# Performance work log

Hardware: AMD Instinct MI355X
Metric: run time of the kernel (lower is better)

The kernel has to match this reference:

```python
import jax, jax.numpy as jnp
import numpy as np

B, H, Wd, CIN = 4, 64, 64, 65   # batch, height, width, in_channels (incl. time)
COUT = 256                      # out_channels (incl. time)
K = 3
KK = K * K
PAD, STRIDE = 1, 1
SOUT = 4                        # output_stabilizer_size (C4 rotations)
CURV = 1.0                      # Lorentz manifold curvature k
LIN_FEAT = (CIN - 1) * KK + 1   # 577


def make_c4_z2_indices(ksize):
    # (out_rotation, in_stabilizer=1, u, v, [s, u_src, v_src]) index table,
    # realizing the C4 filter rotation as a gather (as in GrouPy).
    f = np.arange(ksize * ksize).reshape(ksize, ksize)
    inds = np.zeros((4, 1, ksize, ksize, 3), dtype=np.int64)
    for r in range(4):
        rot = np.rot90(f, r)
        u, v = np.unravel_index(rot, (ksize, ksize))
        inds[r, 0, :, :, 1] = u
        inds[r, 0, :, :, 2] = v
    return inds

INDS = make_c4_z2_indices(K)


def setup_inputs() -> dict:
    key = jax.random.key(0)
    k1, k2, k3 = jax.random.split(key, 3)
    stdv = float(np.sqrt(2.0 / ((CIN - 1) * KK)))  # reset_parameters
    x = jax.random.normal(k1, (B, H, Wd, CIN), dtype=jnp.float32)
    W = jax.random.uniform(k2, (COUT, LIN_FEAT), minval=-stdv, maxval=stdv, dtype=jnp.float32)
    b = jax.random.uniform(k3, (COUT,), minval=-stdv, maxval=stdv, dtype=jnp.float32)
    return {"x": x, "W": W, "b": b}


def _unfold(x):
    # x: (B, C, H, W) -> (B, C*KK, Ho*Wo) in torch.nn.Unfold layout (channel-major, kernel-minor)
    xp = jnp.pad(x, ((0, 0), (0, 0), (PAD, PAD), (PAD, PAD)))
    ho = (H + 2 * PAD - K) // STRIDE + 1
    wo = (Wd + 2 * PAD - K) // STRIDE + 1
    cols = [xp[:, :, i:i + ho * STRIDE:STRIDE, j:j + wo * STRIDE:STRIDE]
            for i in range(K) for j in range(K)]
    p = jnp.stack(cols, axis=2)  # (B, C, KK, ho, wo)
    return p.reshape(B, CIN * KK, ho * wo), ho, wo


def _forward(x, W, b):
    # torch code does x.view(B, C, H, W) on channel-last data: a reshape, not a permute.
    xv = x.reshape(B, CIN, H, Wd)
    patches, ho, wo = _unfold(xv)
    patches = jnp.transpose(patches, (0, 2, 1))          # (B, P, C*KK)
    P = patches.shape[1]
    patches = patches.reshape(B, P, CIN, 1, K, K)
    patches = jnp.broadcast_to(patches, (B, P, CIN, SOUT, K, K))  # repeat over group dim
    # --- group-equivariant filter transform realized as a gather on patches ---
    ir = INDS.reshape(-1, 3)                              # (SOUT*KK, 3)
    pi = patches[:, :, :, ir[:, 0], ir[:, 1], ir[:, 2]]   # (B, P, C, SOUT*KK)
    pi = pi.reshape(B, P, CIN, SOUT, KK)
    pt = jnp.transpose(pi, (3, 0, 1, 2, 4)).reshape(SOUT, B, P, CIN * KK)
    # --- extract_lorentz_patches (vectorized over group dim) ---
    sqrt_k = jnp.sqrt(jnp.float32(CURV))
    t = jnp.maximum(pt[..., :KK], sqrt_k)                 # clamp time components
    t_resc = jnp.sqrt(jnp.sum(t * t, axis=-1, keepdims=True) - (KK - 1) * CURV)
    sp = pt[..., KK:]                                     # (SOUT,B,P,(C-1)*KK) channel-major
    sp = sp.reshape(SOUT, B, P, CIN - 1, KK).swapaxes(-1, -2).reshape(SOUT, B, P, (CIN - 1) * KK)
    pre = jnp.concatenate([t_resc, sp], axis=-1)          # (SOUT,B,P,LIN_FEAT)
    # --- LorentzFullyConnected: linear, then recompute time from space norm ---
    y = jnp.einsum('gbpf,of->gbpo', pre, W) + b           # (SOUT,B,P,COUT)
    y_sp = y[..., 1:]
    y_t = jnp.sqrt(jnp.sum(y_sp * y_sp, axis=-1, keepdims=True) + CURV)
    out = jnp.concatenate([y_t, y_sp], axis=-1)
    out = jnp.transpose(out, (1, 0, 2, 3)).reshape(B, SOUT, ho, wo, COUT)
    return out


def reference(x, W, b):
    return _forward(x, W, b)
```

## Files before the change

### kernel.cpp

```cpp
#include <hip/hip_runtime.h>
#include <hip/hip_bf16.h>

#define CIN 65
#define LIN 577
#define NSTEP 18
#define M_  16384

typedef __bf16 bf16x8 __attribute__((ext_vector_type(8)));
typedef float  f32x4  __attribute__((ext_vector_type(4)));
typedef unsigned short u16x8 __attribute__((ext_vector_type(8)));

__constant__ int SIG[4][9] = {
  {0,1,2,3,4,5,6,7,8},
  {2,5,8,1,4,7,0,3,6},
  {8,7,6,5,4,3,2,1,0},
  {6,3,0,7,4,1,8,5,2}};

__device__ __forceinline__ int swzm(int r) { return (r ^ (r >> 2)) & 3; }

__global__ __launch_bounds__(512) void prep_k(const float* __restrict__ x,
                                              const float* __restrict__ W,
                                              __hip_bfloat16* __restrict__ A,
                                              __hip_bfloat16* __restrict__ Wg,
                                              float* __restrict__ T) {
  __shared__ float lds[CIN * 3 * 72];
  const int tid = threadIdx.x;
  if (blockIdx.x >= 256) {
    int pidx = (blockIdx.x - 256) * 512 + tid;
    int jc  = pidx & 3;
    int col = (pidx >> 2) & 255;
    int t   = pidx >> 10;
    int ks  = t % NSTEP, g = t / NSTEP;
    int k   = SIG[(4 - g) & 3][ks >> 1];
    const float* src = W + col * LIN + 1 + k * 64 + (ks & 1) * 32 + jc * 8;
    u16x8 pk;
#pragma unroll
    for (int e = 0; e < 8; ++e) {
      union { __hip_bfloat16 h; unsigned short u; } cv;
      cv.h = __float2bfloat16(src[e]);
      pk[e] = cv.u;
    }
    *(u16x8*)(Wg + (size_t)pidx * 8) = pk;
    return;
  }
  const int b = blockIdx.x >> 6, py = blockIdx.x & 63;
  const float* xb = x + (size_t)b * (CIN * 4096);
  for (int i = tid; i < CIN * 3 * 18; i += 512)
    *(f32x4*)&lds[i * 4] = (f32x4){0.f, 0.f, 0.f, 0.f};
  __syncthreads();
  for (int i = tid; i < CIN * 3 * 16; i += 512) {
    int pr = i >> 4, j = i & 15;
    int c = pr / 3, dy = pr - c * 3;
    int hy = py + dy - 1;
    if (hy >= 0 && hy < 64)
      *(f32x4*)&lds[c * 216 + dy * 72 + 4 + j * 4] =
          *(const f32x4*)(xb + c * 4096 + hy * 64 + j * 4);
  }
  __syncthreads();

  const int wave = tid >> 6, px = tid & 63;
  const int rowid = (blockIdx.x << 6) | px;
#pragma unroll
  for (int qi = 0; qi < 9; ++qi) {
    int q = wave * 9 + qi;
    int m = q >> 3, cb8 = q & 7;
    int dy = m / 3, dx = m - dy * 3;
    const float* src = &lds[(1 + cb8 * 8) * 216 + dy * 72 + 3 + dx + px];
    u16x8 pk;
#pragma unroll
    for (int e = 0; e < 8; ++e) {
      union { __hip_bfloat16 h; unsigned short u; } cv;
      cv.h = __float2bfloat16(src[e * 216]);
      pk[e] = cv.u;
    }
    *(u16x8*)(A + ((size_t)q * M_ + rowid) * 8) = pk;
  }
  if (wave == 0) {
    float s = 0.f;
#pragma unroll
    for (int m = 0; m < 9; ++m) {
      float t = fmaxf(lds[(m / 3) * 72 + 3 + (m % 3) + px], 1.f);
      s += t * t;
    }
    T[rowid] = sqrtf(s - 8.f);
  }
}

__device__ __forceinline__ void async_cp16(const void* g, void* ldsbase) {
  __builtin_amdgcn_global_load_lds(
      (const __attribute__((address_space(1))) void*)g,
      (__attribute__((address_space(3))) void*)ldsbase, 16, 0, 0);
}

__global__ __launch_bounds__(256, 4) void gemm_k(const __hip_bfloat16* __restrict__ A,
                                                 const __hip_bfloat16* __restrict__ Wg,
                                                 const float* __restrict__ W,
                                                 const float* __restrict__ bias,
                                                 const float* __restrict__ T,
                                                 float* __restrict__ out) {
  __shared__ __align__(16) char smem[32768];
  const int g = blockIdx.x >> 8, rb = blockIdx.x & 255;
  const int brow = rb << 6;
  const int tid = threadIdx.x, wave = tid >> 6, lane = tid & 63;
  const int fr = lane & 15, fq = lane >> 4;
  const int wcb = wave * 64;

  const int bc  = tid >> 2;
  const __hip_bfloat16* Wgg = Wg + ((size_t)(g * NSTEP) << 13);
  auto STAGE_B = [&](char* pb, int ks) {
    const __hip_bfloat16* bs = Wgg + ((size_t)ks << 13);
#pragma unroll
    for (int l = 0; l < 4; ++l) {
      int c = l * 64 + bc;
      int lc = (tid & 3) ^ swzm(c);
      async_cp16(bs + c * 32 + lc * 8, pb + (l * 256 + wave * 64) * 16);
    }
  };
  const __hip_bfloat16* Alane = A + (((size_t)fq * M_ + brow + fr) << 3);
  bf16x8 af[4];
  auto LOAD_A = [&](int ks) {
#pragma unroll
    for (int i = 0; i < 4; ++i)
      af[i] = *(const bf16x8*)(Alane + (size_t)ks * (M_ * 32) + i * 128);
  };

  f32x4 acc[4][4] = {};
  auto COMPUTE = [&](const char* Bb) {
    bf16x8 bf[4];
#pragma unroll
    for (int j = 0; j < 4; ++j) {
      int c = wcb + j * 16 + fr;
      bf[j] = *(const bf16x8*)(Bb + c * 64 + ((fq ^ swzm(c)) << 4));
    }
    __builtin_amdgcn_s_setprio(1);
#pragma unroll
    for (int i = 0; i < 4; ++i)
#pragma unroll
      for (int j = 0; j < 4; ++j)
        acc[i][j] = __builtin_amdgcn_mfma_f32_16x16x32_bf16(af[i], bf[j], acc[i][j], 0, 0, 0);
    __builtin_amdgcn_s_setprio(0);
  };

  STAGE_B(smem, 0);
  for (int ks = 0; ks < NSTEP; ++ks) {
    LOAD_A(ks);
    asm volatile("s_waitcnt vmcnt(4)" ::: "memory");
    __builtin_amdgcn_s_barrier();
    if (ks + 1 < NSTEP) STAGE_B(smem + ((ks + 1) & 1) * 16384, ks + 1);
    COMPUTE(smem + (ks & 1) * 16384);
  }
  __syncthreads();

  float* Ps = (float*)smem;
  float bo[4], w0v[4]; int oc[4];
#pragma unroll
  for (int j = 0; j < 4; ++j) {
    oc[j]  = wcb + j * 16 + fr;
    bo[j]  = bias[oc[j]];
    w0v[j] = W[oc[j] * LIN];
  }
#pragma unroll
  for (int i = 0; i < 4; ++i) {
#pragma unroll
    for (int rr = 0; rr < 4; ++rr) {
      int rl = i * 16 + fq * 4 + rr;
      int row = brow + rl;
      size_t obase = ((size_t)(((row >> 12) * 4 + g) * 4096 + (row & 4095)) << 8);
      float tval = T[row];
      float s = 0.f;
#pragma unroll
      for (int j = 0; j < 4; ++j) {
        float y = acc[i][j][rr] + bo[j] + tval * w0v[j];
        if (oc[j] != 0) { s += y * y; out[obase + oc[j]] = y; }
      }
      s += __shfl_xor(s, 1); s += __shfl_xor(s, 2);
      s += __shfl_xor(s, 4); s += __shfl_xor(s, 8);
      if (fr == 0) Ps[rl * 4 + wave] = s;
    }
  }
  __syncthreads();
  if (tid < 64) {
    int row = brow + tid;
    float s = Ps[tid * 4] + Ps[tid * 4 + 1] + Ps[tid * 4 + 2] + Ps[tid * 4 + 3] + 1.0f;
    out[(size_t)(((row >> 12) * 4 + g) * 4096 + (row & 4095)) << 8] = sqrtf(s);
  }
}

extern "C" void kernel_launch(void* const* d_in, const int* in_sizes, int n_in,
                              void* d_out, int out_size, void* d_ws, size_t ws_size,
                              hipStream_t stream) {
  const float* x    = (const float*)d_in[0];
  const float* W    = (const float*)d_in[1];
  const float* bias = (const float*)d_in[2];
  float* out = (float*)d_out;

  char* ws = (char*)d_ws;
  __hip_bfloat16* Wg = (__hip_bfloat16*)ws;
  float*          T  = (float*)(ws + 1179648);
  __hip_bfloat16* A  = (__hip_bfloat16*)(ws + 1245184);

  prep_k<<<400, 512, 0, stream>>>(x, W, A, Wg, T);
  gemm_k<<<1024, 256, 0, stream>>>(A, Wg, W, bias, T, out);
}
```

Before: 46.33 us.

## Fuse im2col into GEMM via LDS-staged input rows, stream weights from registers

Removes the materialized im2col buffer A and the T buffer. Each GEMM block now loads three input rows of x into LDS as swizzled bf16 and builds the A fragments from there, computing the time rescale locally. Weight fragments are loaded straight from global into double-buffered registers instead of async LDS staging. This drops a large global write and read of the patch matrix. In exchange each block redoes the x staging, and with g as the outer index of the block id the same input rows are staged four times, once per rotation.

```diff
diff --git a/kernel.cpp b/kernel.cpp
--- a/kernel.cpp
+++ b/kernel.cpp
@@ -16,122 +16,101 @@
   {8,7,6,5,4,3,2,1,0},
   {6,3,0,7,4,1,8,5,2}};
 
-__device__ __forceinline__ int swzm(int r) { return (r ^ (r >> 2)) & 3; }
+__global__ __launch_bounds__(512) void prep_w(const float* __restrict__ W,
+                                              __hip_bfloat16* __restrict__ Wg) {
+  int pidx = blockIdx.x * 512 + threadIdx.x;
+  int k8  = pidx & 3;
+  int col = (pidx >> 2) & 255;
+  int t   = pidx >> 10;
+  int ks  = t % NSTEP, g = t / NSTEP;
+  int k   = SIG[(4 - g) & 3][ks >> 1];
+  const float* src = W + col * LIN + 1 + k * 64 + (ks & 1) * 32 + k8 * 8;
+  u16x8 pk;
+#pragma unroll
+  for (int e = 0; e < 8; ++e) {
+    union { __hip_bfloat16 h; unsigned short u; } cv;
+    cv.h = __float2bfloat16(src[e]);
+    pk[e] = cv.u;
+  }
+  *(u16x8*)(Wg + (size_t)pidx * 8) = pk;
+}
 
-__global__ __launch_bounds__(512) void prep_k(const float* __restrict__ x,
-                                              const float* __restrict__ W,
-                                              __hip_bfloat16* __restrict__ A,
-                                              __hip_bfloat16* __restrict__ Wg,
-                                              float* __restrict__ T) {
-  __shared__ float lds[CIN * 3 * 72];
-  const int tid = threadIdx.x;
-  if (blockIdx.x >= 256) {
-    int pidx = (blockIdx.x - 256) * 512 + tid;
-    int jc  = pidx & 3;
-    int col = (pidx >> 2) & 255;
-    int t   = pidx >> 10;
-    int ks  = t % NSTEP, g = t / NSTEP;
-    int k   = SIG[(4 - g) & 3][ks >> 1];
-    const float* src = W + col * LIN + 1 + k * 64 + (ks & 1) * 32 + jc * 8;
-    u16x8 pk;
+__global__ __launch_bounds__(256) void fused_k(const float* __restrict__ x,
+                                               const __hip_bfloat16* __restrict__ Wg,
+                                               const float* __restrict__ W,
+                                               const float* __restrict__ bias,
+                                               float* __restrict__ out) {
+  __shared__ __align__(16) char smem[28768];
+  __hip_bfloat16* xs = (__hip_bfloat16*)smem;
+  float* x0  = (float*)(smem + 27648);
+  float* Tsh = (float*)(smem + 28512);
+
+  const int fid = blockIdx.x;
+  const int g = fid >> 8, bp = fid & 255;
+  const int b = bp >> 6, py = bp & 63;
+  const int tid = threadIdx.x, wave = tid >> 6, lane = tid & 63;
+  const int fr = lane & 15, fq = lane >> 4;
+  const int wcb = wave * 64;
+  const int brow = bp << 6;
+
+  const __hip_bfloat16* Wgg = Wg + (((size_t)g * NSTEP) << 13)
+                                 + (size_t)(wcb + fr) * 32 + fq * 8;
+  bf16x8 pA[4], pB[4];
+  auto LOADB = [&](bf16x8* dst, int ks) {
 #pragma unroll
-    for (int e = 0; e < 8; ++e) {
-      union { __hip_bfloat16 h; unsigned short u; } cv;
-      cv.h = __float2bfloat16(src[e]);
-      pk[e] = cv.u;
+    for (int j = 0; j < 4; ++j)
+      dst[j] = *(const bf16x8*)(Wgg + ((size_t)ks << 13) + j * 512);
+  };
+  LOADB(pA, 0);
+
+  for (int i = tid; i < 1782; i += 256)
+    *(f32x4*)(smem + i * 16) = (f32x4){0.f, 0.f, 0.f, 0.f};
+  __syncthreads();
+
+  const float* xb = x + (size_t)b * (CIN * 4096);
+#pragma unroll
+  for (int r = 0; r < 12; ++r) {
+    int idx = r * 256 + tid;
+    int qq = idx >> 4, v4 = idx & 15;
+    int c1 = qq / 3, hyi = qq - c1 * 3;
+    int hy = py + hyi - 1;
+    if (hy >= 0 && hy < 64) {
+      f32x4 v = *(const f32x4*)(xb + (1 + c1) * 4096 + hy * 64 + v4 * 4);
+#pragma unroll
+      for (int e = 0; e < 4; ++e) {
+        int s = 4 + v4 * 4 + e;
+        xs[(hyi * 72 + s) * 64 + (((c1 >> 3) ^ (s & 7)) << 3) + (c1 & 7)] =
+            __float2bfloat16(v[e]);
+      }
     }
-    *(u16x8*)(Wg + (size_t)pidx * 8) = pk;
-    return;
   }
-  const int b = blockIdx.x >> 6, py = blockIdx.x & 63;
-  const float* xb = x + (size_t)b * (CIN * 4096);
-  for (int i = tid; i < CIN * 3 * 18; i += 512)
-    *(f32x4*)&lds[i * 4] = (f32x4){0.f, 0.f, 0.f, 0.f};
-  __syncthreads();
-  for (int i = tid; i < CIN * 3 * 16; i += 512) {
-    int pr = i >> 4, j = i & 15;
-    int c = pr / 3, dy = pr - c * 3;
-    int hy = py + dy - 1;
+  if (tid < 48) {
+    int hyi = tid >> 4, v4 = tid & 15;
+    int hy = py + hyi - 1;
     if (hy >= 0 && hy < 64)
-      *(f32x4*)&lds[c * 216 + dy * 72 + 4 + j * 4] =
-          *(const f32x4*)(xb + c * 4096 + hy * 64 + j * 4);
+      *(f32x4*)&x0[hyi * 72 + 4 + v4 * 4] = *(const f32x4*)(xb + hy * 64 + v4 * 4);
   }
   __syncthreads();
-
-  const int wave = tid >> 6, px = tid & 63;
-  const int rowid = (blockIdx.x << 6) | px;
-#pragma unroll
-  for (int qi = 0; qi < 9; ++qi) {
-    int q = wave * 9 + qi;
-    int m = q >> 3, cb8 = q & 7;
-    int dy = m / 3, dx = m - dy * 3;
-    const float* src = &lds[(1 + cb8 * 8) * 216 + dy * 72 + 3 + dx + px];
-    u16x8 pk;
-#pragma unroll
-    for (int e = 0; e < 8; ++e) {
-      union { __hip_bfloat16 h; unsigned short u; } cv;
-      cv.h = __float2bfloat16(src[e * 216]);
-      pk[e] = cv.u;
-    }
-    *(u16x8*)(A + ((size_t)q * M_ + rowid) * 8) = pk;
-  }
-  if (wave == 0) {
+  if (tid < 64) {
     float s = 0.f;
 #pragma unroll
     for (int m = 0; m < 9; ++m) {
-      float t = fmaxf(lds[(m / 3) * 72 + 3 + (m % 3) + px], 1.f);
-      s += t * t;
+      float tv = fmaxf(x0[(m / 3) * 72 + 3 + tid + (m % 3)], 1.f);
+      s += tv * tv;
     }
-    T[rowid] = sqrtf(s - 8.f);
+    Tsh[tid] = sqrtf(s - 8.f);
   }
-}
 
-__device__ __forceinline__ void async_cp16(const void* g, void* ldsbase) {
-  __builtin_amdgcn_global_load_lds(
-      (const __attribute__((address_space(1))) void*)g,
-      (__attribute__((address_space(3))) void*)ldsbase, 16, 0, 0);
-}
-
-__global__ __launch_bounds__(256, 4) void gemm_k(const __hip_bfloat16* __restrict__ A,
-                                                 const __hip_bfloat16* __restrict__ Wg,
-                                                 const float* __restrict__ W,
-                                                 const float* __restrict__ bias,
-                                                 const float* __restrict__ T,
-                                                 float* __restrict__ out) {
-  __shared__ __align__(16) char smem[32768];
-  const int g = blockIdx.x >> 8, rb = blockIdx.x & 255;
-  const int brow = rb << 6;
-  const int tid = threadIdx.x, wave = tid >> 6, lane = tid & 63;
-  const int fr = lane & 15, fq = lane >> 4;
-  const int wcb = wave * 64;
-
-  const int bc  = tid >> 2;
-  const __hip_bfloat16* Wgg = Wg + ((size_t)(g * NSTEP) << 13);
-  auto STAGE_B = [&](char* pb, int ks) {
-    const __hip_bfloat16* bs = Wgg + ((size_t)ks << 13);
-#pragma unroll
-    for (int l = 0; l < 4; ++l) {
-      int c = l * 64 + bc;
-      int lc = (tid & 3) ^ swzm(c);
-      async_cp16(bs + c * 32 + lc * 8, pb + (l * 256 + wave * 64) * 16);
-    }
-  };
-  const __hip_bfloat16* Alane = A + (((size_t)fq * M_ + brow + fr) << 3);
-  bf16x8 af[4];
-  auto LOAD_A = [&](int ks) {
+  f32x4 acc[4][4] = {};
+  auto COMPUTE = [&](int ks, const bf16x8* bf) {
+    const int m = ks >> 1, dy = m / 3, dx = m % 3;
+    const int sb = 3 + fr + dx;
+    const int pc = ((ks & 1) * 4 + fq) ^ (sb & 7);
+    const char* base = smem + ((dy * 72 + sb) * 8 + pc) * 16;
+    bf16x8 af[4];
 #pragma unroll
     for (int i = 0; i < 4; ++i)
-      af[i] = *(const bf16x8*)(Alane + (size_t)ks * (M_ * 32) + i * 128);
-  };
-
-  f32x4 acc[4][4] = {};
-  auto COMPUTE = [&](const char* Bb) {
-    bf16x8 bf[4];
-#pragma unroll
-    for (int j = 0; j < 4; ++j) {
-      int c = wcb + j * 16 + fr;
-      bf[j] = *(const bf16x8*)(Bb + c * 64 + ((fq ^ swzm(c)) << 4));
-    }
+      af[i] = *(const bf16x8*)(base + i * 2048);
     __builtin_amdgcn_s_setprio(1);
 #pragma unroll
     for (int i = 0; i < 4; ++i)
@@ -141,13 +120,12 @@
     __builtin_amdgcn_s_setprio(0);
   };
 
-  STAGE_B(smem, 0);
-  for (int ks = 0; ks < NSTEP; ++ks) {
-    LOAD_A(ks);
-    asm volatile("s_waitcnt vmcnt(4)" ::: "memory");
-    __builtin_amdgcn_s_barrier();
-    if (ks + 1 < NSTEP) STAGE_B(smem + ((ks + 1) & 1) * 16384, ks + 1);
-    COMPUTE(smem + (ks & 1) * 16384);
+#pragma unroll
+  for (int kp = 0; kp < NSTEP; kp += 2) {
+    LOADB(pB, kp + 1);
+    COMPUTE(kp, pA);
+    if (kp + 2 < NSTEP) LOADB(pA, kp + 2);
+    COMPUTE(kp + 1, pB);
   }
   __syncthreads();
 
@@ -166,7 +144,7 @@
       int rl = i * 16 + fq * 4 + rr;
       int row = brow + rl;
       size_t obase = ((size_t)(((row >> 12) * 4 + g) * 4096 + (row & 4095)) << 8);
-      float tval = T[row];
+      float tval = Tsh[rl];
       float s = 0.f;
 #pragma unroll
       for (int j = 0; j < 4; ++j) {
@@ -194,11 +172,8 @@
   const float* bias = (const float*)d_in[2];
   float* out = (float*)d_out;
 
-  char* ws = (char*)d_ws;
-  __hip_bfloat16* Wg = (__hip_bfloat16*)ws;
-  float*          T  = (float*)(ws + 1179648);
-  __hip_bfloat16* A  = (__hip_bfloat16*)(ws + 1245184);
+  __hip_bfloat16* Wg = (__hip_bfloat16*)d_ws;
 
-  prep_k<<<400, 512, 0, stream>>>(x, W, A, Wg, T);
-  gemm_k<<<1024, 256, 0, stream>>>(A, Wg, W, bias, T, out);
+  prep_w <<<144, 512, 0, stream>>>(W, Wg);
+  fused_k<<<1024, 256, 0, stream>>>(x, Wg, W, bias, out);
 }
```

Result: slower. 51.69 us (+11.6%).
